# Performance work log

Hardware: AMD Instinct MI355X
Metric: run time of the kernel (lower is better)

The kernel has to match this reference:

```python
import jax, jax.numpy as jnp
import numpy as np
import math

B, T, C = 4, 1024, 1024
H = 16          # n_head
E = 8           # num_experts
K = 2           # top_k
HID = 4096      # expert_hidden_dim
TEMP = 1.0
EPS_LN = 1e-5


def setup_inputs() -> dict:
    key = jax.random.key(0)
    ks = jax.random.split(key, 16)
    s = 0.02
    return {
        'x': jax.random.normal(ks[0], (B, T, C), jnp.float32),
        'ln1_g': jnp.ones((C,), jnp.float32),
        'ln1_b': jnp.zeros((C,), jnp.float32),
        'W_qkv': jax.random.normal(ks[1], (C, 3 * C), jnp.float32) * s,
        'b_qkv': jnp.zeros((3 * C,), jnp.float32),
        'W_proj': jax.random.normal(ks[2], (C, C), jnp.float32) * s,
        'b_proj': jnp.zeros((C,), jnp.float32),
        'ln2_g': jnp.ones((C,), jnp.float32),
        'ln2_b': jnp.zeros((C,), jnp.float32),
        'W_router': jax.random.normal(ks[3], (C, E), jnp.float32) * s,
        'W1': jax.random.normal(ks[4], (E, C, HID), jnp.float32) * s,
        'b1': jnp.zeros((E, HID), jnp.float32),
        'W2': jax.random.normal(ks[5], (E, HID, C), jnp.float32) * s,
        'b2': jnp.zeros((E, C), jnp.float32),
    }


def _layernorm(x, g, b):
    mu = jnp.mean(x, axis=-1, keepdims=True)
    var = jnp.mean(jnp.square(x - mu), axis=-1, keepdims=True)
    return (x - mu) * jax.lax.rsqrt(var + EPS_LN) * g + b


def reference(x, ln1_g, ln1_b, W_qkv, b_qkv, W_proj, b_proj,
              ln2_g, ln2_b, W_router, W1, b1, W2, b2):
    D = C // H
    # --- causal self-attention on ln_1(x) ---
    h = _layernorm(x, ln1_g, ln1_b)
    qkv = h @ W_qkv + b_qkv                      # [B,T,3C]
    q, k, v = jnp.split(qkv, 3, axis=-1)
    q = q.reshape(B, T, H, D).transpose(0, 2, 1, 3)   # [B,H,T,D]
    k = k.reshape(B, T, H, D).transpose(0, 2, 1, 3)
    v = v.reshape(B, T, H, D).transpose(0, 2, 1, 3)
    att = jnp.einsum('bhqd,bhkd->bhqk', q, k) * (1.0 / math.sqrt(D))
    mask = jnp.tril(jnp.ones((T, T), bool))
    att = jnp.where(mask, att, -jnp.inf)
    att = jax.nn.softmax(att, axis=-1)
    y = jnp.einsum('bhqk,bhkd->bhqd', att, v)
    y = y.transpose(0, 2, 1, 3).reshape(B, T, C)
    x = x + (y @ W_proj + b_proj)

    # --- sparse MoE on ln_2(x) ---
    h2 = _layernorm(x, ln2_g, ln2_b)
    xf = h2.reshape(-1, C)                       # [N,C]
    N = xf.shape[0]
    logits = (xf @ W_router) / TEMP              # [N,E]
    prob = jax.nn.softmax(logits, axis=-1)
    top_prob, top_idx = jax.lax.top_k(prob, K)   # [N,K]
    top_prob = top_prob / (jnp.sum(top_prob, axis=-1, keepdims=True) + 1e-9)
    # dense per-token per-expert combine weights (0 for unselected experts)
    w = jnp.zeros((N, E), xf.dtype).at[jnp.arange(N)[:, None], top_idx].add(top_prob)
    # dense expert compute (weights zero out unselected experts -> same math)
    hid = jax.nn.gelu(jnp.einsum('nc,ech->neh', xf, W1) + b1, approximate=False)
    eo = jnp.einsum('neh,ehc->nec', hid, W2) + b2          # [N,E,C]
    out_flat = jnp.einsum('nec,ne->nc', eo, w)
    x = x + out_flat.reshape(B, T, C)

    counts = jnp.zeros((E,), jnp.float32).at[top_idx.reshape(-1)].add(1.0)
    expert_utilization = counts / (jnp.sum(counts) + 1e-9)
    return x, expert_utilization
```

## Files before the change

### kernel.cpp

```cpp
#include <hip/hip_runtime.h>
#include <cmath>

#define CDIM 1024
#define NTOK 4096
#define NHEAD 16
#define HDIM 64
#define NEXP 8
#define HIDD 4096
#define MAXROWS 9216

typedef short bf16x8 __attribute__((ext_vector_type(8)));
typedef short s16x4  __attribute__((ext_vector_type(4)));
typedef float f32x4  __attribute__((ext_vector_type(4)));

static __device__ __forceinline__ short f2bf(float f){
  unsigned u = __builtin_bit_cast(unsigned, f);
  u += 0x7fffu + ((u >> 16) & 1u);
  return (short)(u >> 16);
}

static __device__ __forceinline__ int swz64(int r, int ch){
  return r*64 + (((ch ^ (r>>1)) & 3) << 4);
}
static __device__ __forceinline__ int swz128(int r, int ch){
  return r*128 + (((ch ^ r) & 7) << 4);
}

static __device__ __forceinline__ void gl16(const short* g, short* l){
  __builtin_amdgcn_global_load_lds(
      (const __attribute__((address_space(1))) void*)g,
      (__attribute__((address_space(3))) void*)l, 16, 0, 0);
}

__global__ void k_transpose_cast(const float* __restrict__ in, short* __restrict__ out,
                                 int R, int Cc){
  __shared__ float tile[64][65];
  const int z = blockIdx.z;
  const float* src = in + (long long)z*R*Cc;
  short* dst = out + (long long)z*R*Cc;
  const int r0 = blockIdx.y*64, c0 = blockIdx.x*64;
  const int t = threadIdx.x;
  #pragma unroll
  for (int it=0; it<4; ++it){
    const int item = t + it*256;
    const int r = item>>4, c4 = item&15;
    const float4 v = *(const float4*)(src + (long long)(r0+r)*Cc + c0 + c4*4);
    tile[r][c4*4+0]=v.x; tile[r][c4*4+1]=v.y; tile[r][c4*4+2]=v.z; tile[r][c4*4+3]=v.w;
  }
  __syncthreads();
  #pragma unroll
  for (int it=0; it<2; ++it){
    const int item = t + it*256;
    const int rr8 = item & 7, cc = item >> 3;
    bf16x8 o;
    #pragma unroll
    for (int i=0;i<8;i++) o[i] = f2bf(tile[rr8*8+i][cc]);
    *(bf16x8*)(dst + (long long)(c0+cc)*R + r0 + rr8*8) = o;
  }
}

__global__ void k_ln1(const float* __restrict__ x, const float* __restrict__ g,
                      const float* __restrict__ b, short* __restrict__ out){
  const int row = blockIdx.x;
  const int t = threadIdx.x;
  const float4 v = ((const float4*)(x + (long long)row*CDIM))[t];
  float s  = v.x+v.y+v.z+v.w;
  float s2 = v.x*v.x+v.y*v.y+v.z*v.z+v.w*v.w;
  #pragma unroll
  for (int mm=1; mm<64; mm<<=1){ s += __shfl_xor(s,mm); s2 += __shfl_xor(s2,mm); }
  __shared__ float ps[4], ps2[4];
  const int w = t>>6, l = t&63;
  if (l==0){ ps[w]=s; ps2[w]=s2; }
  __syncthreads();
  s  = ps[0]+ps[1]+ps[2]+ps[3];
  s2 = ps2[0]+ps2[1]+ps2[2]+ps2[3];
  const float mu = s*(1.f/CDIM);
  const float rstd = rsqrtf(s2*(1.f/CDIM) - mu*mu + 1e-5f);
  const float4 gg = ((const float4*)g)[t];
  const float4 bb = ((const float4*)b)[t];
  s16x4 o;
  o[0]=f2bf((v.x-mu)*rstd*gg.x+bb.x); o[1]=f2bf((v.y-mu)*rstd*gg.y+bb.y);
  o[2]=f2bf((v.z-mu)*rstd*gg.z+bb.z); o[3]=f2bf((v.w-mu)*rstd*gg.w+bb.w);
  *(s16x4*)(out + (long long)row*CDIM + t*4) = o;
}

__global__ void k_ln2_router(const float* __restrict__ x1, const float* __restrict__ g,
                             const float* __restrict__ b, const float* __restrict__ Wr,
                             short* __restrict__ h2, int* __restrict__ tidx,
                             float* __restrict__ tw, int* __restrict__ counts){
  const int row = blockIdx.x;
  const int t = threadIdx.x;
  const float4 v = ((const float4*)(x1 + (long long)row*CDIM))[t];
  float s  = v.x+v.y+v.z+v.w;
  float s2 = v.x*v.x+v.y*v.y+v.z*v.z+v.w*v.w;
  #pragma unroll
  for (int mm=1; mm<64; mm<<=1){ s += __shfl_xor(s,mm); s2 += __shfl_xor(s2,mm); }
  __shared__ float ps[4], ps2[4];
  const int w = t>>6, l = t&63;
  if (l==0){ ps[w]=s; ps2[w]=s2; }
  __syncthreads();
  s  = ps[0]+ps[1]+ps[2]+ps[3];
  s2 = ps2[0]+ps2[1]+ps2[2]+ps2[3];
  const float mu = s*(1.f/CDIM);
  const float rstd = rsqrtf(s2*(1.f/CDIM) - mu*mu + 1e-5f);
  const float4 gg = ((const float4*)g)[t];
  const float4 bb = ((const float4*)b)[t];
  const float y0=(v.x-mu)*rstd*gg.x+bb.x, y1=(v.y-mu)*rstd*gg.y+bb.y;
  const float y2=(v.z-mu)*rstd*gg.z+bb.z, y3=(v.w-mu)*rstd*gg.w+bb.w;
  s16x4 o; o[0]=f2bf(y0); o[1]=f2bf(y1); o[2]=f2bf(y2); o[3]=f2bf(y3);
  *(s16x4*)(h2 + (long long)row*CDIM + t*4) = o;

  float acc[8];
  const float* wr0 = Wr + (long long)(t*4)*NEXP;
  #pragma unroll
  for (int e=0;e<8;e++) acc[e] = y0*wr0[e] + y1*wr0[8+e] + y2*wr0[16+e] + y3*wr0[24+e];
  #pragma unroll
  for (int mm=1; mm<64; mm<<=1){
    #pragma unroll
    for (int e=0;e<8;e++) acc[e] += __shfl_xor(acc[e], mm);
  }
  __shared__ float pl[4][8];
  if (l==0){
    #pragma unroll
    for (int e=0;e<8;e++) pl[w][e]=acc[e];
  }
  __syncthreads();
  if (t==0){
    float lg[8];
    #pragma unroll
    for (int e=0;e<8;e++) lg[e] = pl[0][e]+pl[1][e]+pl[2][e]+pl[3][e];
    float mx = lg[0];
    #pragma unroll
    for (int e=1;e<8;e++) mx = fmaxf(mx, lg[e]);
    float pr[8]; float sum = 0.f;
    #pragma unroll
    for (int e=0;e<8;e++){ pr[e]=expf(lg[e]-mx); sum += pr[e]; }
    int i0 = 0;
    #pragma unroll
    for (int e=1;e<8;e++) if (pr[e] > pr[i0]) i0 = e;
    int i1 = (i0==0) ? 1 : 0;
    #pragma unroll
    for (int e=0;e<8;e++) if (e!=i0 && pr[e] > pr[i1]) i1 = e;
    const float p0 = pr[i0]/sum, p1 = pr[i1]/sum;
    const float dn = p0 + p1 + 1e-9f;
    tidx[row*2]=i0; tidx[row*2+1]=i1;
    tw[row*2]=p0/dn; tw[row*2+1]=p1/dn;
    atomicAdd(&counts[i0],1); atomicAdd(&counts[i1],1);
  }
}

__global__ void k_route_setup(const int* __restrict__ counts, int* __restrict__ offs,
                              int* __restrict__ cursors, int* __restrict__ rowmap,
                              float* __restrict__ util){
  if (threadIdx.x == 0){
    int o = 0;
    for (int e=0;e<8;e++){
      offs[e] = o; cursors[e] = o;
      o += (counts[e] + 127) & ~127;
    }
    offs[8] = o;
    for (int e=0;e<8;e++) util[e] = (float)counts[e] / 8192.0f;
  }
  for (int i = threadIdx.x; i < MAXROWS; i += blockDim.x) rowmap[i] = -1;
}

__global__ void k_scatter(const int* __restrict__ tidx, const float* __restrict__ tw,
                          int* __restrict__ cursors, int* __restrict__ rowmap,
                          float* __restrict__ roww, int* __restrict__ posmap){
  const int i = blockIdx.x*blockDim.x + threadIdx.x;
  if (i >= 2*NTOK) return;
  const int e = tidx[i];
  const int pos = atomicAdd(&cursors[e], 1);
  rowmap[pos] = i >> 1;
  roww[pos]   = tw[i];
  posmap[i]   = pos;
}

template<int EPI>
__launch_bounds__(512, 4)
__global__ void k_gemm(const short* __restrict__ A, const short* __restrict__ Bt,
                       const float* __restrict__ bias, const float* __restrict__ resid,
                       void* __restrict__ Cout, int N, int K,
                       const int* __restrict__ rowmap, const int* __restrict__ offs,
                       long long expStrideB, const short* __restrict__ zrow){
  int wg = blockIdx.x;
  const int nwg = gridDim.x;
  {
    const int q = nwg >> 3, r8 = nwg & 7;
    const int xcd = wg & 7, pos = wg >> 3;
    wg = (xcd < r8 ? xcd*(q+1) : r8*(q+1) + (xcd - r8)*q) + pos;
  }
  const int gridN = N >> 7;
  const int gridM = nwg / gridN;
  const int mtile = wg % gridM, ntile = wg / gridM;
  const int mbase = mtile*128;
  const int nbase = ntile*128;
  int e = 0;
  if constexpr (EPI >= 2){
    if (mbase >= offs[8]) return;
    while (e < 7 && mbase >= offs[e+1]) e++;
    Bt += (long long)e * expStrideB;
  }
  __shared__ short Asm[2][4096];
  __shared__ short Bsm[2][4096];
  const int tid = threadIdx.x;
  const int w = tid >> 6, l = tid & 63;
  const int wr = w >> 1, wc = w & 1;
  const int l15 = l & 15, l4 = l >> 4;

  const short* aSrc; const short* bSrc;
  {
    const int r = tid >> 2, ch = tid & 3;
    const int sch = (ch ^ (r >> 1)) & 3;
    if constexpr (EPI == 2){
      const int grow = rowmap[mbase + r];
      aSrc = (grow >= 0) ? (A + (long long)grow*K + sch*8) : (zrow + sch*8);
    } else {
      aSrc = A + (long long)(mbase + r)*K + sch*8;
    }
    bSrc = Bt + (long long)(nbase + r)*K + sch*8;
  }
  const int dOff = w*512;

  f32x4 acc[2][4];
  const f32x4 z4 = {0.f,0.f,0.f,0.f};
  #pragma unroll
  for (int i=0;i<2;i++){
    #pragma unroll
    for (int jn=0;jn<4;jn++) acc[i][jn] = z4;
  }

  auto stage = [&](int buf, int kt){
    gl16(aSrc + kt, &Asm[buf][dOff]);
    gl16(bSrc + kt, &Bsm[buf][dOff]);
  };
  auto compute = [&](int buf){
    bf16x8 af[2], bfr[4];
    #pragma unroll
    for (int i=0;i<2;i++)
      af[i]  = *(const bf16x8*)((char*)Asm[buf] + swz64(wr*32 + i*16 + l15, l4));
    #pragma unroll
    for (int jn=0;jn<4;jn++)
      bfr[jn] = *(const bf16x8*)((char*)Bsm[buf] + swz64(wc*64 + jn*16 + l15, l4));
    __builtin_amdgcn_s_setprio(1);
    #pragma unroll
    for (int i=0;i<2;i++){
      #pragma unroll
      for (int jn=0;jn<4;jn++)
        acc[i][jn] = __builtin_amdgcn_mfma_f32_16x16x32_bf16(af[i], bfr[jn], acc[i][jn], 0,0,0);
    }
    __builtin_amdgcn_s_setprio(0);
  };

  stage(0, 0);
  asm volatile("s_waitcnt vmcnt(0)" ::: "memory");
  __builtin_amdgcn_s_barrier();

  int cur = 0;
  for (int kt = 32; kt < K; kt += 32){
    stage(cur ^ 1, kt);
    compute(cur);
    asm volatile("s_waitcnt vmcnt(0)" ::: "memory");
    __builtin_amdgcn_s_barrier();
    cur ^= 1;
  }
  compute(cur);

  #pragma unroll
  for (int i=0;i<2;i++){
    const int row0 = mbase + wr*32 + i*16 + l4*4;
    #pragma unroll
    for (int jn=0;jn<4;jn++){
      const int col = nbase + wc*64 + jn*16 + l15;
      const float bi = bias[(EPI>=2 ? e*N : 0) + col];
      #pragma unroll
      for (int j=0;j<4;j++){
        const long long idx = (long long)(row0 + j)*N + col;
        float v = acc[i][jn][j] + bi;
        if constexpr (EPI == 0){
          ((short*)Cout)[idx] = f2bf(v);
        } else if constexpr (EPI == 1){
          ((float*)Cout)[idx] = v + resid[idx];
        } else if constexpr (EPI == 2){
          ((short*)Cout)[idx] = f2bf(0.5f*v*(1.0f + erff(v*0.70710678118654752f)));
        } else {
          ((float*)Cout)[idx] = v;
        }
      }
    }
  }
}

__launch_bounds__(256)
__global__ void k_attn(const short* __restrict__ qkv, short* __restrict__ y){
  const int qt = blockIdx.x;
  const int bh = blockIdx.y;
  const int bb = bh >> 4;
  const int h  = bh & 15;
  const int tid = threadIdx.x;
  const int w = tid >> 6, l = tid & 63;
  const int l15 = l & 15, l4 = l >> 4;

  __shared__ short Ksm[64*64];
  __shared__ short Vtsm[64*64];
  __shared__ short Psm[4*16*64];

  const long long rs = 3*CDIM;
  const int qrow0 = bb*1024 + qt*64;

  bf16x8 aq[2];
  {
    const int qr = qrow0 + w*16 + l15;
    const short* qp = qkv + (long long)qr*rs + h*HDIM;
    aq[0] = *(const bf16x8*)(qp + l4*8);
    aq[1] = *(const bf16x8*)(qp + 32 + l4*8);
  }

  const f32x4 z4 = {0.f,0.f,0.f,0.f};
  f32x4 O[4];
  #pragma unroll
  for (int cf=0;cf<4;cf++) O[cf] = z4;
  float mrow[4], lrow[4];
  #pragma unroll
  for (int j=0;j<4;j++){ mrow[j] = -1e30f; lrow[j] = 0.f; }

  for (int kvb = 0; kvb <= qt; ++kvb){
    const int kvrow0 = bb*1024 + kvb*64;
    #pragma unroll
    for (int p=0;p<2;p++){
      const int ch = tid + p*256;
      const int r = ch >> 3, c = ch & 7;
      const short* kp = qkv + (long long)(kvrow0 + r)*rs + CDIM + h*HDIM + c*8;
      *(bf16x8*)((char*)Ksm + swz128(r, c)) = *(const bf16x8*)kp;
      const short* vp = qkv + (long long)(kvrow0 + r)*rs + 2*CDIM + h*HDIM + c*8;
      bf16x8 vv = *(const bf16x8*)vp;
      const int off2 = 2*r;
      const int g0 = off2 >> 4, b0 = off2 & 15;
      #pragma unroll
      for (int i=0;i<8;i++){
        const int d = c*8 + i;
        *(short*)((char*)Vtsm + d*128 + (((g0 ^ d) & 7) << 4) + b0) = vv[i];
      }
    }
    __syncthreads();

    f32x4 S[4];
    #pragma unroll
    for (int cf=0;cf<4;cf++) S[cf] = z4;
    #pragma unroll
    for (int cf=0;cf<4;cf++){
      #pragma unroll
      for (int kf=0;kf<2;kf++){
        bf16x8 bk = *(const bf16x8*)((char*)Ksm + swz128(cf*16 + l15, kf*4 + l4));
        S[cf] = __builtin_amdgcn_mfma_f32_16x16x32_bf16(aq[kf], bk, S[cf], 0,0,0);
      }
    }

    const bool diag = (kvb == qt);
    #pragma unroll
    for (int cf=0;cf<4;cf++){
      #pragma unroll
      for (int j=0;j<4;j++){
        float s = S[cf][j] * 0.125f;
        if (diag && (cf*16 + l15 > w*16 + l4*4 + j)) s = -1e30f;
        S[cf][j] = s;
      }
    }

    float alpha[4];
    #pragma unroll
    for (int j=0;j<4;j++){
      float mx = fmaxf(fmaxf(S[0][j],S[1][j]), fmaxf(S[2][j],S[3][j]));
      #pragma unroll
      for (int mm=1; mm<16; mm<<=1) mx = fmaxf(mx, __shfl_xor(mx, mm));
      const float mnew = fmaxf(mrow[j], mx);
      const float al = expf(mrow[j] - mnew);
      float psum = 0.f;
      #pragma unroll
      for (int cf=0;cf<4;cf++){ float pp = expf(S[cf][j]-mnew); S[cf][j]=pp; psum += pp; }
      #pragma unroll
      for (int mm=1; mm<16; mm<<=1) psum += __shfl_xor(psum, mm);
      lrow[j] = lrow[j]*al + psum;
      mrow[j] = mnew; alpha[j] = al;
    }
    #pragma unroll
    for (int cf=0;cf<4;cf++){
      #pragma unroll
      for (int j=0;j<4;j++) O[cf][j] *= alpha[j];
    }

    char* pw = (char*)Psm + w*2048;
    #pragma unroll
    for (int cf=0;cf<4;cf++){
      #pragma unroll
      for (int j=0;j<4;j++){
        const int r = l4*4 + j;
        const int cb = (cf*16 + l15)*2;
        *(short*)(pw + r*128 + ((((cb>>4) ^ r) & 7)<<4) + (cb & 15)) = f2bf(S[cf][j]);
      }
    }
    bf16x8 pa[2];
    pa[0] = *(const bf16x8*)(pw + swz128(l15, l4));
    pa[1] = *(const bf16x8*)(pw + swz128(l15, 4 + l4));
    #pragma unroll
    for (int cf=0;cf<4;cf++){
      #pragma unroll
      for (int kf=0;kf<2;kf++){
        bf16x8 bv = *(const bf16x8*)((char*)Vtsm + swz128(cf*16 + l15, kf*4 + l4));
        O[cf] = __builtin_amdgcn_mfma_f32_16x16x32_bf16(pa[kf], bv, O[cf], 0,0,0);
      }
    }
    __syncthreads();
  }

  const int yr0 = qrow0 + w*16;
  #pragma unroll
  for (int cf=0;cf<4;cf++){
    #pragma unroll
    for (int j=0;j<4;j++){
      const int r = l4*4 + j;
      y[(long long)(yr0 + r)*CDIM + h*HDIM + cf*16 + l15] = f2bf(O[cf][j] / lrow[j]);
    }
  }
}

__global__ void k_combine(const float* __restrict__ x1, const float* __restrict__ eo,
                          const int* __restrict__ posmap, const float* __restrict__ roww,
                          float* __restrict__ out){
  const int row = blockIdx.x;
  const int t = threadIdx.x;
  const int p0 = posmap[row*2], p1 = posmap[row*2+1];
  const float w0 = roww[p0], w1 = roww[p1];
  const float4 a  = ((const float4*)(x1 + (long long)row*CDIM))[t];
  const float4 e0 = ((const float4*)(eo + (long long)p0*CDIM))[t];
  const float4 e1 = ((const float4*)(eo + (long long)p1*CDIM))[t];
  float4 r;
  r.x = a.x + w0*e0.x + w1*e1.x;
  r.y = a.y + w0*e0.y + w1*e1.y;
  r.z = a.z + w0*e0.z + w1*e1.z;
  r.w = a.w + w0*e0.w + w1*e1.w;
  ((float4*)(out + (long long)row*CDIM))[t] = r;
}

extern "C" void kernel_launch(void* const* d_in, const int* in_sizes, int n_in,
                              void* d_out, int out_size, void* d_ws, size_t ws_size,
                              hipStream_t stream){
  const float* x     = (const float*)d_in[0];
  const float* ln1_g = (const float*)d_in[1];
  const float* ln1_b = (const float*)d_in[2];
  const float* W_qkv = (const float*)d_in[3];
  const float* b_qkv = (const float*)d_in[4];
  const float* W_proj= (const float*)d_in[5];
  const float* b_proj= (const float*)d_in[6];
  const float* ln2_g = (const float*)d_in[7];
  const float* ln2_b = (const float*)d_in[8];
  const float* W_r   = (const float*)d_in[9];
  const float* W1    = (const float*)d_in[10];
  const float* b1    = (const float*)d_in[11];
  const float* W2    = (const float*)d_in[12];
  const float* b2    = (const float*)d_in[13];
  float* out = (float*)d_out;
  float* util = out + (long long)NTOK*CDIM;

  char* p = (char*)d_ws;
  auto alloc = [&](size_t bytes)->char*{
    char* r = p; p += (bytes + 255) & ~(size_t)255; return r;
  };
  short* Wt1   = (short*)alloc((size_t)NEXP*HIDD*CDIM*2);
  short* Wt2   = (short*)alloc((size_t)NEXP*CDIM*HIDD*2);
  float* x1    = (float*)alloc((size_t)NTOK*CDIM*4);
  short* h2    = (short*)alloc((size_t)NTOK*CDIM*2);
  short* hid   = (short*)alloc((size_t)MAXROWS*HIDD*2);
  int*   tidx  = (int*)alloc(2*NTOK*4);
  float* tw    = (float*)alloc(2*NTOK*4);
  int*   counts= (int*)alloc(256);
  int*   offs  = (int*)alloc(256);
  int*   curs  = (int*)alloc(256);
  int*   rowmap= (int*)alloc(MAXROWS*4);
  float* roww  = (float*)alloc(MAXROWS*4);
  int*   posmap= (int*)alloc(2*NTOK*4);
  short* zrow  = (short*)alloc(8192);
  char* transStart = p;
  short* WtQ = (short*)alloc((size_t)3*CDIM*CDIM*2);
  short* WtP = (short*)alloc((size_t)CDIM*CDIM*2);
  short* h   = (short*)alloc((size_t)NTOK*CDIM*2);
  short* qkv = (short*)alloc((size_t)NTOK*3*CDIM*2);
  short* y   = (short*)alloc((size_t)NTOK*CDIM*2);
  float* eo  = (float*)transStart;

  (void)hipMemsetAsync(counts, 0, 32, stream);
  (void)hipMemsetAsync(zrow, 0, 8192, stream);

  k_transpose_cast<<<dim3(3*CDIM/64, CDIM/64, 1), 256, 0, stream>>>(W_qkv, WtQ, CDIM, 3*CDIM);
  k_transpose_cast<<<dim3(CDIM/64, CDIM/64, 1),   256, 0, stream>>>(W_proj, WtP, CDIM, CDIM);
  k_transpose_cast<<<dim3(HIDD/64, CDIM/64, NEXP),256, 0, stream>>>(W1, Wt1, CDIM, HIDD);
  k_transpose_cast<<<dim3(CDIM/64, HIDD/64, NEXP),256, 0, stream>>>(W2, Wt2, HIDD, CDIM);

  k_ln1<<<NTOK, 256, 0, stream>>>(x, ln1_g, ln1_b, h);

  k_gemm<0><<<dim3((NTOK/128)*(3*CDIM/128)), 512, 0, stream>>>(
      h, WtQ, b_qkv, nullptr, qkv, 3*CDIM, CDIM, nullptr, nullptr, 0, nullptr);

  k_attn<<<dim3(1024/64, 4*NHEAD), 256, 0, stream>>>(qkv, y);

  k_gemm<1><<<dim3((NTOK/128)*(CDIM/128)), 512, 0, stream>>>(
      y, WtP, b_proj, x, x1, CDIM, CDIM, nullptr, nullptr, 0, nullptr);

  k_ln2_router<<<NTOK, 256, 0, stream>>>(x1, ln2_g, ln2_b, W_r, h2, tidx, tw, counts);
  k_route_setup<<<1, 256, 0, stream>>>(counts, offs, curs, rowmap, util);
  k_scatter<<<(2*NTOK)/256, 256, 0, stream>>>(tidx, tw, curs, rowmap, roww, posmap);

  k_gemm<2><<<dim3((MAXROWS/128)*(HIDD/128)), 512, 0, stream>>>(
      h2, Wt1, b1, nullptr, hid, HIDD, CDIM, rowmap, offs, (long long)HIDD*CDIM, zrow);
  k_gemm<3><<<dim3((MAXROWS/128)*(CDIM/128)), 512, 0, stream>>>(
      hid, Wt2, b2, nullptr, eo, CDIM, HIDD, nullptr, offs, (long long)CDIM*HIDD, zrow);

  k_combine<<<NTOK, 256, 0, stream>>>(x1, eo, posmap, roww, out);
}
```

Baseline: 653.0 us.

## Add 256x256-tile GEMM with split-phase pipelining for QKV and expert GEMMs

Introduces a new GEMM kernel with 256x256 output tiles, 8 waves each computing 128x64, and a 64-wide K step split into four load/compute phases with prefetch interleaved and s_setprio around the MFMAs. It is used for the QKV projection and both expert GEMMs. Expert padding moves to 256-row alignment, which raises MAXROWS. The old kernel is kept only for the attention output projection with the residual add. The larger tiles increase data reuse per load and cut global/LDS traffic. In exchange they add more padded rows per expert, use more LDS and registers (occupancy drops to 2 blocks), and launch fewer workgroups.

```diff
diff --git a/kernel.cpp b/kernel.cpp
--- a/kernel.cpp
+++ b/kernel.cpp
@@ -7,7 +7,7 @@
 #define HDIM 64
 #define NEXP 8
 #define HIDD 4096
-#define MAXROWS 9216
+#define MAXROWS 10240
 
 typedef short bf16x8 __attribute__((ext_vector_type(8)));
 typedef short s16x4  __attribute__((ext_vector_type(4)));
@@ -156,7 +156,7 @@
     int o = 0;
     for (int e=0;e<8;e++){
       offs[e] = o; cursors[e] = o;
-      o += (counts[e] + 127) & ~127;
+      o += (counts[e] + 255) & ~255;
     }
     offs[8] = o;
     for (int e=0;e<8;e++) util[e] = (float)counts[e] / 8192.0f;
@@ -177,12 +177,12 @@
 }
 
 template<int EPI>
-__launch_bounds__(512, 4)
-__global__ void k_gemm(const short* __restrict__ A, const short* __restrict__ Bt,
-                       const float* __restrict__ bias, const float* __restrict__ resid,
-                       void* __restrict__ Cout, int N, int K,
-                       const int* __restrict__ rowmap, const int* __restrict__ offs,
-                       long long expStrideB, const short* __restrict__ zrow){
+__launch_bounds__(512, 2)
+__global__ void k_gemm_big(const short* __restrict__ A, const short* __restrict__ Bt,
+                           const float* __restrict__ bias, void* __restrict__ Cout,
+                           int N, int K, const int* __restrict__ rowmap,
+                           const int* __restrict__ offs, long long expStrideB,
+                           const short* __restrict__ zrow){
   int wg = blockIdx.x;
   const int nwg = gridDim.x;
   {
@@ -190,17 +190,143 @@
     const int xcd = wg & 7, pos = wg >> 3;
     wg = (xcd < r8 ? xcd*(q+1) : r8*(q+1) + (xcd - r8)*q) + pos;
   }
+  const int gridN = N >> 8;
+  const int gridM = nwg / gridN;
+  const int mtile = wg % gridM, ntile = wg / gridM;
+  const int mbase = mtile*256, nbase = ntile*256;
+  int e = 0;
+  if constexpr (EPI >= 2){
+    if (mbase >= offs[8]) return;
+    while (e < 7 && mbase >= offs[e+1]) e++;
+    Bt += (long long)e * expStrideB;
+  }
+  __shared__ short Asm[2][2][8192];
+  __shared__ short Bsm[2][2][8192];
+  const int tid = threadIdx.x;
+  const int w = tid >> 6, l = tid & 63;
+  const int wr = w >> 2, wc = w & 3;
+  const int l15 = l & 15, l4 = l >> 4;
+
+  const short* aS[2]; const short* bS[2]; int ldsOff[2];
+  #pragma unroll
+  for (int inst=0; inst<2; ++inst){
+    const int g = inst*512 + tid;
+    const int r = g >> 2, ch = g & 3;
+    const int sch = (ch ^ (r >> 1)) & 3;
+    if constexpr (EPI == 2){
+      const int grow = rowmap[mbase + r];
+      aS[inst] = (grow >= 0) ? (A + (long long)grow*K + sch*8) : (zrow + sch*8);
+    } else {
+      aS[inst] = A + (long long)(mbase + r)*K + sch*8;
+    }
+    bS[inst] = Bt + (long long)(nbase + r)*K + sch*8;
+    ldsOff[inst] = inst*4096 + w*512;
+  }
+
+  f32x4 acc[8][4];
+  const f32x4 z4 = {0.f,0.f,0.f,0.f};
+  #pragma unroll
+  for (int m=0;m<8;m++){
+    #pragma unroll
+    for (int n=0;n<4;n++) acc[m][n] = z4;
+  }
+
+  auto stage = [&](int p, int buf, int kt){
+    const int ks = p >> 1;
+    if (!(p & 1)){
+      #pragma unroll
+      for (int inst=0; inst<2; ++inst)
+        gl16(aS[inst] + kt + ks*32, &Asm[buf][ks][ldsOff[inst]]);
+    } else {
+      #pragma unroll
+      for (int inst=0; inst<2; ++inst)
+        gl16(bS[inst] + kt + ks*32, &Bsm[buf][ks][ldsOff[inst]]);
+    }
+  };
+
+  const int nt = K >> 6;
+  stage(0, 0, 0); stage(1, 0, 0); stage(2, 0, 0); stage(3, 0, 0);
+  asm volatile("s_waitcnt vmcnt(0)" ::: "memory");
+  __syncthreads();
+
+  bf16x8 bfr[4];
+  for (int t = 0; t < nt; ++t){
+    const int buf = t & 1;
+    const int ktn = (t + 1) << 6;
+    const bool pre = (t + 1 < nt);
+    #pragma unroll
+    for (int p = 0; p < 4; ++p){
+      const int ks = p >> 1;
+      if (p == 0 || p == 2){
+        #pragma unroll
+        for (int n=0;n<4;n++)
+          bfr[n] = *(const bf16x8*)((const char*)Bsm[buf][ks] + swz64(wc*64 + n*16 + l15, l4));
+      }
+      bf16x8 af[4];
+      #pragma unroll
+      for (int mi=0; mi<4; mi++){
+        const int m = (p&1)*4 + mi;
+        af[mi] = *(const bf16x8*)((const char*)Asm[buf][ks] + swz64(wr*128 + m*16 + l15, l4));
+      }
+      if (pre){
+        stage(p, buf^1, ktn);
+        asm volatile("s_waitcnt vmcnt(4)" ::: "memory");
+      } else if (p == 1){
+        asm volatile("s_waitcnt vmcnt(0)" ::: "memory");
+      }
+      __builtin_amdgcn_s_barrier();
+      __builtin_amdgcn_s_setprio(1);
+      #pragma unroll
+      for (int mi=0; mi<4; mi++){
+        const int m = (p&1)*4 + mi;
+        #pragma unroll
+        for (int n=0;n<4;n++)
+          acc[m][n] = __builtin_amdgcn_mfma_f32_16x16x32_bf16(af[mi], bfr[n], acc[m][n], 0,0,0);
+      }
+      __builtin_amdgcn_s_setprio(0);
+      __builtin_amdgcn_s_barrier();
+    }
+  }
+
+  #pragma unroll
+  for (int m=0;m<8;m++){
+    const int row0 = mbase + wr*128 + m*16 + l4*4;
+    #pragma unroll
+    for (int n=0;n<4;n++){
+      const int col = nbase + wc*64 + n*16 + l15;
+      const float bi = bias[(EPI>=2 ? e*N : 0) + col];
+      #pragma unroll
+      for (int j=0;j<4;j++){
+        const long long idx = (long long)(row0 + j)*N + col;
+        float v = acc[m][n][j] + bi;
+        if constexpr (EPI == 0){
+          ((short*)Cout)[idx] = f2bf(v);
+        } else if constexpr (EPI == 2){
+          ((short*)Cout)[idx] = f2bf(0.5f*v*(1.0f + erff(v*0.70710678118654752f)));
+        } else {
+          ((float*)Cout)[idx] = v;
+        }
+      }
+    }
+  }
+}
+
+__launch_bounds__(512, 4)
+__global__ void k_gemm(const short* __restrict__ A, const short* __restrict__ Bt,
+                       const float* __restrict__ bias, const float* __restrict__ resid,
+                       float* __restrict__ Cout, int N, int K){
+  int wg = blockIdx.x;
+  const int nwg = gridDim.x;
+  {
+    const int q = nwg >> 3, r8 = nwg & 7;
+    const int xcd = wg & 7, pos = wg >> 3;
+    wg = (xcd < r8 ? xcd*(q+1) : r8*(q+1) + (xcd - r8)*q) + pos;
+  }
   const int gridN = N >> 7;
   const int gridM = nwg / gridN;
   const int mtile = wg % gridM, ntile = wg / gridM;
   const int mbase = mtile*128;
   const int nbase = ntile*128;
-  int e = 0;
-  if constexpr (EPI >= 2){
-    if (mbase >= offs[8]) return;
-    while (e < 7 && mbase >= offs[e+1]) e++;
-    Bt += (long long)e * expStrideB;
-  }
   __shared__ short Asm[2][4096];
   __shared__ short Bsm[2][4096];
   const int tid = threadIdx.x;
@@ -212,12 +338,7 @@
   {
     const int r = tid >> 2, ch = tid & 3;
     const int sch = (ch ^ (r >> 1)) & 3;
-    if constexpr (EPI == 2){
-      const int grow = rowmap[mbase + r];
-      aSrc = (grow >= 0) ? (A + (long long)grow*K + sch*8) : (zrow + sch*8);
-    } else {
-      aSrc = A + (long long)(mbase + r)*K + sch*8;
-    }
+    aSrc = A + (long long)(mbase + r)*K + sch*8;
     bSrc = Bt + (long long)(nbase + r)*K + sch*8;
   }
   const int dOff = w*512;
@@ -272,20 +393,11 @@
     #pragma unroll
     for (int jn=0;jn<4;jn++){
       const int col = nbase + wc*64 + jn*16 + l15;
-      const float bi = bias[(EPI>=2 ? e*N : 0) + col];
+      const float bi = bias[col];
       #pragma unroll
       for (int j=0;j<4;j++){
         const long long idx = (long long)(row0 + j)*N + col;
-        float v = acc[i][jn][j] + bi;
-        if constexpr (EPI == 0){
-          ((short*)Cout)[idx] = f2bf(v);
-        } else if constexpr (EPI == 1){
-          ((float*)Cout)[idx] = v + resid[idx];
-        } else if constexpr (EPI == 2){
-          ((short*)Cout)[idx] = f2bf(0.5f*v*(1.0f + erff(v*0.70710678118654752f)));
-        } else {
-          ((float*)Cout)[idx] = v;
-        }
+        Cout[idx] = acc[i][jn][j] + bi + resid[idx];
       }
     }
   }
@@ -498,22 +610,22 @@
 
   k_ln1<<<NTOK, 256, 0, stream>>>(x, ln1_g, ln1_b, h);
 
-  k_gemm<0><<<dim3((NTOK/128)*(3*CDIM/128)), 512, 0, stream>>>(
-      h, WtQ, b_qkv, nullptr, qkv, 3*CDIM, CDIM, nullptr, nullptr, 0, nullptr);
+  k_gemm_big<0><<<dim3((NTOK/256)*(3*CDIM/256)), 512, 0, stream>>>(
+      h, WtQ, b_qkv, qkv, 3*CDIM, CDIM, nullptr, nullptr, 0, nullptr);
 
   k_attn<<<dim3(1024/64, 4*NHEAD), 256, 0, stream>>>(qkv, y);
 
-  k_gemm<1><<<dim3((NTOK/128)*(CDIM/128)), 512, 0, stream>>>(
-      y, WtP, b_proj, x, x1, CDIM, CDIM, nullptr, nullptr, 0, nullptr);
+  k_gemm<<<dim3((NTOK/128)*(CDIM/128)), 512, 0, stream>>>(
+      y, WtP, b_proj, x, x1, CDIM, CDIM);
 
   k_ln2_router<<<NTOK, 256, 0, stream>>>(x1, ln2_g, ln2_b, W_r, h2, tidx, tw, counts);
   k_route_setup<<<1, 256, 0, stream>>>(counts, offs, curs, rowmap, util);
   k_scatter<<<(2*NTOK)/256, 256, 0, stream>>>(tidx, tw, curs, rowmap, roww, posmap);
 
-  k_gemm<2><<<dim3((MAXROWS/128)*(HIDD/128)), 512, 0, stream>>>(
-      h2, Wt1, b1, nullptr, hid, HIDD, CDIM, rowmap, offs, (long long)HIDD*CDIM, zrow);
-  k_gemm<3><<<dim3((MAXROWS/128)*(CDIM/128)), 512, 0, stream>>>(
-      hid, Wt2, b2, nullptr, eo, CDIM, HIDD, nullptr, offs, (long long)CDIM*HIDD, zrow);
+  k_gemm_big<2><<<dim3((MAXROWS/256)*(HIDD/256)), 512, 0, stream>>>(
+      h2, Wt1, b1, hid, HIDD, CDIM, rowmap, offs, (long long)HIDD*CDIM, zrow);
+  k_gemm_big<3><<<dim3((MAXROWS/256)*(CDIM/256)), 512, 0, stream>>>(
+      hid, Wt2, b2, eo, CDIM, HIDD, nullptr, offs, (long long)CDIM*HIDD, zrow);
 
   k_combine<<<NTOK, 256, 0, stream>>>(x1, eo, posmap, roww, out);
 }
```

Result: no change. 665.2 us (+1.9%).

## Process two query tiles per attention block to share K/V tile loads

Applied to the files above, without the earlier changes.

The attention kernel now uses 512-thread blocks, each covering 128 query rows split into two 64-row halves. Every K/V tile staged in shared memory serves both halves, which halves global K/V traffic and transpose work per query row. The cost is fewer blocks (512 instead of 1024) and idle waves in the lower half on the final diagonal tile. Each block also still walks a causal range of uneven length.

```diff
diff --git a/kernel.cpp b/kernel.cpp
--- a/kernel.cpp
+++ b/kernel.cpp
@@ -291,29 +291,32 @@
   }
 }
 
-__launch_bounds__(256)
+__launch_bounds__(512)
 __global__ void k_attn(const short* __restrict__ qkv, short* __restrict__ y){
-  const int qt = blockIdx.x;
+  const int qp = blockIdx.x;
   const int bh = blockIdx.y;
   const int bb = bh >> 4;
   const int h  = bh & 15;
   const int tid = threadIdx.x;
   const int w = tid >> 6, l = tid & 63;
+  const int half = w >> 2, wq = w & 3;
   const int l15 = l & 15, l4 = l >> 4;
 
   __shared__ short Ksm[64*64];
   __shared__ short Vtsm[64*64];
-  __shared__ short Psm[4*16*64];
+  __shared__ short Psm[8*16*64];
 
   const long long rs = 3*CDIM;
-  const int qrow0 = bb*1024 + qt*64;
+  const int qrow0 = bb*1024 + qp*128;
+  const int myQt = (qp << 1) + half;
+  const int qtHigh = (qp << 1) + 1;
 
   bf16x8 aq[2];
   {
-    const int qr = qrow0 + w*16 + l15;
-    const short* qp = qkv + (long long)qr*rs + h*HDIM;
-    aq[0] = *(const bf16x8*)(qp + l4*8);
-    aq[1] = *(const bf16x8*)(qp + 32 + l4*8);
+    const int qr = qrow0 + half*64 + wq*16 + l15;
+    const short* qp2 = qkv + (long long)qr*rs + h*HDIM;
+    aq[0] = *(const bf16x8*)(qp2 + l4*8);
+    aq[1] = *(const bf16x8*)(qp2 + 32 + l4*8);
   }
 
   const f32x4 z4 = {0.f,0.f,0.f,0.f};
@@ -324,12 +327,10 @@
   #pragma unroll
   for (int j=0;j<4;j++){ mrow[j] = -1e30f; lrow[j] = 0.f; }
 
-  for (int kvb = 0; kvb <= qt; ++kvb){
+  for (int kvb = 0; kvb <= qtHigh; ++kvb){
     const int kvrow0 = bb*1024 + kvb*64;
-    #pragma unroll
-    for (int p=0;p<2;p++){
-      const int ch = tid + p*256;
-      const int r = ch >> 3, c = ch & 7;
+    {
+      const int r = tid >> 3, c = tid & 7;
       const short* kp = qkv + (long long)(kvrow0 + r)*rs + CDIM + h*HDIM + c*8;
       *(bf16x8*)((char*)Ksm + swz128(r, c)) = *(const bf16x8*)kp;
       const short* vp = qkv + (long long)(kvrow0 + r)*rs + 2*CDIM + h*HDIM + c*8;
@@ -344,76 +345,78 @@
     }
     __syncthreads();
 
-    f32x4 S[4];
-    #pragma unroll
-    for (int cf=0;cf<4;cf++) S[cf] = z4;
-    #pragma unroll
-    for (int cf=0;cf<4;cf++){
-      #pragma unroll
-      for (int kf=0;kf<2;kf++){
-        bf16x8 bk = *(const bf16x8*)((char*)Ksm + swz128(cf*16 + l15, kf*4 + l4));
-        S[cf] = __builtin_amdgcn_mfma_f32_16x16x32_bf16(aq[kf], bk, S[cf], 0,0,0);
-      }
-    }
-
-    const bool diag = (kvb == qt);
-    #pragma unroll
-    for (int cf=0;cf<4;cf++){
+    if (kvb <= myQt){
+      f32x4 S[4];
+      #pragma unroll
+      for (int cf=0;cf<4;cf++) S[cf] = z4;
+      #pragma unroll
+      for (int cf=0;cf<4;cf++){
+        #pragma unroll
+        for (int kf=0;kf<2;kf++){
+          bf16x8 bk = *(const bf16x8*)((char*)Ksm + swz128(cf*16 + l15, kf*4 + l4));
+          S[cf] = __builtin_amdgcn_mfma_f32_16x16x32_bf16(aq[kf], bk, S[cf], 0,0,0);
+        }
+      }
+
+      const bool diag = (kvb == myQt);
+      #pragma unroll
+      for (int cf=0;cf<4;cf++){
+        #pragma unroll
+        for (int j=0;j<4;j++){
+          float s = S[cf][j] * 0.125f;
+          if (diag && (cf*16 + l15 > wq*16 + l4*4 + j)) s = -1e30f;
+          S[cf][j] = s;
+        }
+      }
+
+      float alpha[4];
       #pragma unroll
       for (int j=0;j<4;j++){
-        float s = S[cf][j] * 0.125f;
-        if (diag && (cf*16 + l15 > w*16 + l4*4 + j)) s = -1e30f;
-        S[cf][j] = s;
-      }
-    }
-
-    float alpha[4];
-    #pragma unroll
-    for (int j=0;j<4;j++){
-      float mx = fmaxf(fmaxf(S[0][j],S[1][j]), fmaxf(S[2][j],S[3][j]));
-      #pragma unroll
-      for (int mm=1; mm<16; mm<<=1) mx = fmaxf(mx, __shfl_xor(mx, mm));
-      const float mnew = fmaxf(mrow[j], mx);
-      const float al = expf(mrow[j] - mnew);
-      float psum = 0.f;
-      #pragma unroll
-      for (int cf=0;cf<4;cf++){ float pp = expf(S[cf][j]-mnew); S[cf][j]=pp; psum += pp; }
-      #pragma unroll
-      for (int mm=1; mm<16; mm<<=1) psum += __shfl_xor(psum, mm);
-      lrow[j] = lrow[j]*al + psum;
-      mrow[j] = mnew; alpha[j] = al;
-    }
-    #pragma unroll
-    for (int cf=0;cf<4;cf++){
-      #pragma unroll
-      for (int j=0;j<4;j++) O[cf][j] *= alpha[j];
-    }
-
-    char* pw = (char*)Psm + w*2048;
-    #pragma unroll
-    for (int cf=0;cf<4;cf++){
-      #pragma unroll
-      for (int j=0;j<4;j++){
-        const int r = l4*4 + j;
-        const int cb = (cf*16 + l15)*2;
-        *(short*)(pw + r*128 + ((((cb>>4) ^ r) & 7)<<4) + (cb & 15)) = f2bf(S[cf][j]);
-      }
-    }
-    bf16x8 pa[2];
-    pa[0] = *(const bf16x8*)(pw + swz128(l15, l4));
-    pa[1] = *(const bf16x8*)(pw + swz128(l15, 4 + l4));
-    #pragma unroll
-    for (int cf=0;cf<4;cf++){
-      #pragma unroll
-      for (int kf=0;kf<2;kf++){
-        bf16x8 bv = *(const bf16x8*)((char*)Vtsm + swz128(cf*16 + l15, kf*4 + l4));
-        O[cf] = __builtin_amdgcn_mfma_f32_16x16x32_bf16(pa[kf], bv, O[cf], 0,0,0);
+        float mx = fmaxf(fmaxf(S[0][j],S[1][j]), fmaxf(S[2][j],S[3][j]));
+        #pragma unroll
+        for (int mm=1; mm<16; mm<<=1) mx = fmaxf(mx, __shfl_xor(mx, mm));
+        const float mnew = fmaxf(mrow[j], mx);
+        const float al = expf(mrow[j] - mnew);
+        float psum = 0.f;
+        #pragma unroll
+        for (int cf=0;cf<4;cf++){ float pp = expf(S[cf][j]-mnew); S[cf][j]=pp; psum += pp; }
+        #pragma unroll
+        for (int mm=1; mm<16; mm<<=1) psum += __shfl_xor(psum, mm);
+        lrow[j] = lrow[j]*al + psum;
+        mrow[j] = mnew; alpha[j] = al;
+      }
+      #pragma unroll
+      for (int cf=0;cf<4;cf++){
+        #pragma unroll
+        for (int j=0;j<4;j++) O[cf][j] *= alpha[j];
+      }
+
+      char* pw = (char*)Psm + w*2048;
+      #pragma unroll
+      for (int cf=0;cf<4;cf++){
+        #pragma unroll
+        for (int j=0;j<4;j++){
+          const int r = l4*4 + j;
+          const int cb = (cf*16 + l15)*2;
+          *(short*)(pw + r*128 + ((((cb>>4) ^ r) & 7)<<4) + (cb & 15)) = f2bf(S[cf][j]);
+        }
+      }
+      bf16x8 pa[2];
+      pa[0] = *(const bf16x8*)(pw + swz128(l15, l4));
+      pa[1] = *(const bf16x8*)(pw + swz128(l15, 4 + l4));
+      #pragma unroll
+      for (int cf=0;cf<4;cf++){
+        #pragma unroll
+        for (int kf=0;kf<2;kf++){
+          bf16x8 bv = *(const bf16x8*)((char*)Vtsm + swz128(cf*16 + l15, kf*4 + l4));
+          O[cf] = __builtin_amdgcn_mfma_f32_16x16x32_bf16(pa[kf], bv, O[cf], 0,0,0);
+        }
       }
     }
     __syncthreads();
   }
 
-  const int yr0 = qrow0 + w*16;
+  const int yr0 = qrow0 + half*64 + wq*16;
   #pragma unroll
   for (int cf=0;cf<4;cf++){
     #pragma unroll
@@ -501,7 +504,7 @@
   k_gemm<0><<<dim3((NTOK/128)*(3*CDIM/128)), 512, 0, stream>>>(
       h, WtQ, b_qkv, nullptr, qkv, 3*CDIM, CDIM, nullptr, nullptr, 0, nullptr);
 
-  k_attn<<<dim3(1024/64, 4*NHEAD), 256, 0, stream>>>(qkv, y);
+  k_attn<<<dim3(1024/128, 4*NHEAD), 512, 0, stream>>>(qkv, y);
 
   k_gemm<1><<<dim3((NTOK/128)*(CDIM/128)), 512, 0, stream>>>(
       y, WtP, b_proj, x, x1, CDIM, CDIM, nullptr, nullptr, 0, nullptr);
```

Result: faster. 632.9 us (-3.1%).
